# Optimization experiments

Hardware: AMD Instinct MI355X
Metric: run time of the kernel (lower is better)

Reference implementation:

```python
import jax, jax.numpy as jnp
import numpy as np

HEAD = 16
EPS = 1.1920929e-07  # torch.finfo(float32).eps, used by nn.RMSNorm when eps=None


def _rms(x, g):
    return x * jax.lax.rsqrt(jnp.mean(x * x, axis=-1, keepdims=True) + EPS) * g


def _heads(t):
    b, L, dm = t.shape
    return t.reshape(b, L, HEAD, dm // HEAD).transpose(0, 2, 1, 3)  # b h L d


def setup_inputs() -> dict:
    key = jax.random.key(0)
    ks = jax.random.split(key, 8)
    b, L, dims = 1, 1024, 1024
    s = dims ** -0.5
    x = jax.random.normal(ks[0], (b, L, dims), jnp.float32)
    pt = jax.random.normal(ks[1], (b, L, dims), jnp.float32)
    # additive causal mask (finite large-negative to stay grad-safe)
    mask = jnp.triu(jnp.full((L, L), -1e9, jnp.float32), k=1)
    return {
        "x": x, "pt": pt, "mask": mask,
        "gq": jnp.ones((dims,), jnp.float32),
        "Wq": jax.random.normal(ks[2], (dims, dims), jnp.float32) * s,
        "bq": jnp.zeros((dims,), jnp.float32),
        "gkv": jnp.ones((dims,), jnp.float32),
        "Wkv": jax.random.normal(ks[3], (dims, 2 * dims), jnp.float32) * s,
        "bkv": jnp.zeros((2 * dims,), jnp.float32),
        "gc": jnp.ones((dims,), jnp.float32),
        "Wc": jax.random.normal(ks[4], (dims, dims), jnp.float32) * s,
        "bc": jnp.zeros((dims,), jnp.float32),
        "Wout": jax.random.normal(ks[5], (dims, dims), jnp.float32) * s,
        "bout": jnp.zeros((dims,), jnp.float32),
        "context_window": 16,
    }


def reference(x, pt, mask, gq, Wq, bq, gkv, Wkv, bkv, gc, Wc, bc, Wout, bout, context_window):
    b, L, dims = x.shape
    d = dims // HEAD
    q = _heads(_rms(x, gq) @ Wq + bq)                      # b h L d
    kv = (_rms(x, gkv) @ Wkv + bkv).reshape(b, L, 2, HEAD, d)
    k = kv[:, :, 0].transpose(0, 2, 1, 3)                  # b h L d
    v = kv[:, :, 1].transpose(0, 2, 1, 3)
    c = _heads(_rms(pt, gc) @ Wc + bc)                     # b h L d

    # triplet_scores[i,j] = sum_{t=max(0,min(i,j)-w)}^{min(L,max(i,j)+w)-1} q_i . (k_j * c_t)
    # Vectorize with prefix sums over c: window sum = P[end] - P[start],
    # where end depends only on max(i,j) and start only on min(i,j).
    P = jnp.concatenate([jnp.zeros((b, HEAD, 1, d), x.dtype), jnp.cumsum(c, axis=2)], axis=2)  # b h L+1 d
    idx = jnp.arange(L)
    S = jnp.clip(idx - context_window, 0, L)   # start for min-index
    E = jnp.clip(idx + context_window, 0, L)   # end for max-index
    PE = jnp.take(P, E, axis=2)                # b h L d
    PS = jnp.take(P, S, axis=2)

    U = jnp.einsum('bhid,bhjd->bhij', q, k * PE)        # end from j (i<=j branch)
    V = jnp.einsum('bhid,bhjd->bhij', q * PS, k)        # start from i (i<=j branch)
    U2 = jnp.einsum('bhid,bhjd->bhij', q * PE, k)       # end from i (i>j branch)
    V2 = jnp.einsum('bhid,bhjd->bhij', q, k * PS)       # start from j (i>j branch)
    lower = idx[:, None] <= idx[None, :]
    triplet = jnp.where(lower, U - V, U2 - V2)          # b h L L

    scale = d ** -0.5
    qk = jnp.einsum('bhid,bhjd->bhij', q, k) * scale + triplet + mask[:L, :L]
    attn = jax.nn.softmax(qk, axis=-1)
    wv = jnp.einsum('bhij,bhjd->bhid', attn, v)
    out = wv.transpose(0, 2, 1, 3).reshape(b, L, dims) @ Wout + bout  # dropout p=0.01 is identity at eval
    return out
```

## Files before the change

### kernel.cpp

```cpp
#include <hip/hip_runtime.h>

#define LQ 1024
#define DM 1024


typedef __attribute__((ext_vector_type(8))) short bf16x8;
typedef __attribute__((ext_vector_type(4))) float f32x4;

#define MFMA(a, b, c) __builtin_amdgcn_mfma_f32_16x16x32_bf16((a), (b), (c), 0, 0, 0)
#define WAIT_LDS() __builtin_amdgcn_s_waitcnt(0xC07F)

__device__ __forceinline__ unsigned short f2bf(float x) {
    unsigned int u = __float_as_uint(x);
    return (unsigned short)((u + 0x7FFFu + ((u >> 16) & 1u)) >> 16);
}
__device__ __forceinline__ float bf2f(unsigned short h) {
    return __uint_as_float(((unsigned int)h) << 16);
}
__device__ __forceinline__ void gload16(const void* gp, void* lp) {
    __builtin_amdgcn_global_load_lds(
        (const __attribute__((address_space(1))) void*)gp,
        (__attribute__((address_space(3))) void*)lp, 16, 0, 0);
}
__device__ __forceinline__ void store_split4(unsigned short* ph, unsigned short* pl,
                                             float4 v) {
    unsigned short h0 = f2bf(v.x), h1 = f2bf(v.y), h2 = f2bf(v.z), h3 = f2bf(v.w);
    uint2 a;
    a.x = (unsigned)h0 | ((unsigned)h1 << 16);
    a.y = (unsigned)h2 | ((unsigned)h3 << 16);
    *(uint2*)ph = a;
    unsigned short l0 = f2bf(v.x - bf2f(h0)), l1 = f2bf(v.y - bf2f(h1));
    unsigned short l2 = f2bf(v.z - bf2f(h2)), l3 = f2bf(v.w - bf2f(h3));
    uint2 b;
    b.x = (unsigned)l0 | ((unsigned)l1 << 16);
    b.y = (unsigned)l2 | ((unsigned)l3 << 16);
    *(uint2*)pl = b;
}

__device__ __forceinline__ void rms_body(
    int row, const float* __restrict__ x, const float* __restrict__ pt,
    const float* __restrict__ gq, const float* __restrict__ gkv,
    const float* __restrict__ gc,
    unsigned short* xqn_h, unsigned short* xqn_l,
    unsigned short* xkvn_h, unsigned short* xkvn_l,
    unsigned short* ptn_h, unsigned short* ptn_l)
{
    const int t = threadIdx.x;
    const bool isx = row < LQ;
    const float* src = isx ? (x + (size_t)row * DM)
                           : (pt + (size_t)(row - LQ) * DM);
    float4 v = ((const float4*)src)[t];
    float ss = v.x*v.x + v.y*v.y + v.z*v.z + v.w*v.w;
    #pragma unroll
    for (int o = 32; o > 0; o >>= 1) ss += __shfl_down(ss, o);
    __shared__ float red[4];
    if ((t & 63) == 0) red[t >> 6] = ss;
    __syncthreads();
    const float r = rsqrtf((red[0] + red[1] + red[2] + red[3]) * (1.0f / DM)
                           + 1.1920929e-07f);
    const size_t base = (size_t)(isx ? row : row - LQ) * DM + t * 4;
    if (isx) {
        float4 g1 = ((const float4*)gq)[t];
        float4 g2 = ((const float4*)gkv)[t];
        float4 y1, y2;
        y1.x = v.x*r*g1.x; y1.y = v.y*r*g1.y; y1.z = v.z*r*g1.z; y1.w = v.w*r*g1.w;
        y2.x = v.x*r*g2.x; y2.y = v.y*r*g2.y; y2.z = v.z*r*g2.z; y2.w = v.w*r*g2.w;
        store_split4(xqn_h + base, xqn_l + base, y1);
        store_split4(xkvn_h + base, xkvn_l + base, y2);
    } else {
        float4 g = ((const float4*)gc)[t];
        float4 y;
        y.x = v.x*r*g.x; y.y = v.y*r*g.y; y.z = v.z*r*g.z; y.w = v.w*r*g.w;
        store_split4(ptn_h + base, ptn_l + base, y);
    }
}

__device__ __forceinline__ void wsplit_body(
    const float* __restrict__ in, unsigned short* oh, unsigned short* ol,
    int K, int N, int bx, int by)
{
    __shared__ float T[64 * 65];
    const int t = threadIdx.x;
    const int tx = t & 15, ty = t >> 4;
    const int c0 = bx * 64, r0 = by * 64;
    #pragma unroll
    for (int p = 0; p < 4; ++p) {
        int row = ty + p * 16;
        float4 v = *(const float4*)(in + (size_t)(r0 + row) * N + c0 + tx * 4);
        T[row * 65 + tx * 4 + 0] = v.x;
        T[row * 65 + tx * 4 + 1] = v.y;
        T[row * 65 + tx * 4 + 2] = v.z;
        T[row * 65 + tx * 4 + 3] = v.w;
    }
    __syncthreads();
    #pragma unroll
    for (int p = 0; p < 4; ++p) {
        int n = ty + p * 16;
        float4 w;
        w.x = T[(tx * 4 + 0) * 65 + n];
        w.y = T[(tx * 4 + 1) * 65 + n];
        w.z = T[(tx * 4 + 2) * 65 + n];
        w.w = T[(tx * 4 + 3) * 65 + n];
        size_t o = (size_t)(c0 + n) * K + r0 + tx * 4;
        store_split4(oh + o, ol + o, w);
    }
}

__global__ __launch_bounds__(256) void prep_kernel(
    const float* __restrict__ x, const float* __restrict__ pt,
    const float* __restrict__ gq, const float* __restrict__ gkv,
    const float* __restrict__ gc,
    const float* __restrict__ Wq, const float* __restrict__ Wkv,
    const float* __restrict__ Wc, const float* __restrict__ Wout,
    unsigned short* xqn_h, unsigned short* xqn_l,
    unsigned short* xkvn_h, unsigned short* xkvn_l,
    unsigned short* ptn_h, unsigned short* ptn_l,
    unsigned short* WqT_h, unsigned short* WqT_l,
    unsigned short* WkvT_h, unsigned short* WkvT_l,
    unsigned short* WcT_h, unsigned short* WcT_l,
    unsigned short* WoT_h, unsigned short* WoT_l)
{
    const int b = blockIdx.x;
    if (b < 2048) {
        rms_body(b, x, pt, gq, gkv, gc, xqn_h, xqn_l, xkvn_h, xkvn_l, ptn_h, ptn_l);
    } else if (b < 2304) {
        int s = b - 2048; wsplit_body(Wq, WqT_h, WqT_l, 1024, 1024, s & 15, s >> 4);
    } else if (b < 2816) {
        int s = b - 2304; wsplit_body(Wkv, WkvT_h, WkvT_l, 1024, 2048, s & 31, s >> 5);
    } else if (b < 3072) {
        int s = b - 2816; wsplit_body(Wc, WcT_h, WcT_l, 1024, 1024, s & 15, s >> 4);
    } else {
        int s = b - 3072; wsplit_body(Wout, WoT_h, WoT_l, 1024, 1024, s & 15, s >> 4);
    }
}

__device__ __forceinline__ void gemm3p(
    const unsigned short* __restrict__ Ah, const unsigned short* __restrict__ Al,
    const unsigned short* __restrict__ Bh, const unsigned short* __restrict__ Bl,
    const float* __restrict__ bias, float* __restrict__ out, int N, int mt, int nt)
{
    __shared__ unsigned short sAh[128 * 32], sAl[128 * 32];
    __shared__ unsigned short sBh[64 * 32], sBl[64 * 32];
    const int t = threadIdx.x;
    const int lane = t & 63, w = t >> 6;
    const int wm = w >> 1, wn = w & 1;
    const int n16 = lane & 15, quad = lane >> 4;
    const int srow = t >> 2, scol = (t & 3) * 8;
    f32x4 zero = {0.f, 0.f, 0.f, 0.f};
    f32x4 acc[4][2];
    #pragma unroll
    for (int ms = 0; ms < 4; ++ms)
        #pragma unroll
        for (int ns = 0; ns < 2; ++ns) acc[ms][ns] = zero;

    for (int kt = 0; kt < 32; ++kt) {
        const int k0 = kt * 32;
        __syncthreads();
        #pragma unroll
        for (int p = 0; p < 2; ++p) {
            const size_t ga = (size_t)(mt * 128 + srow + p * 64) * 1024 + k0 + scol;
            const int lb = w * 512 + p * 2048;
            gload16(Ah + ga, sAh + lb);
            gload16(Al + ga, sAl + lb);
        }
        {
            const size_t gb = (size_t)(nt * 64 + srow) * 1024 + k0 + scol;
            gload16(Bh + gb, sBh + w * 512);
            gload16(Bl + gb, sBl + w * 512);
        }
        __syncthreads();
        bf16x8 afh[4], afl[4], bfh[2], bfl[2];
        #pragma unroll
        for (int ms = 0; ms < 4; ++ms) {
            int r = wm * 64 + ms * 16 + n16;
            afh[ms] = *(const bf16x8*)&sAh[r * 32 + quad * 8];
            afl[ms] = *(const bf16x8*)&sAl[r * 32 + quad * 8];
        }
        #pragma unroll
        for (int ns = 0; ns < 2; ++ns) {
            int r = wn * 32 + ns * 16 + n16;
            bfh[ns] = *(const bf16x8*)&sBh[r * 32 + quad * 8];
            bfl[ns] = *(const bf16x8*)&sBl[r * 32 + quad * 8];
        }
        #pragma unroll
        for (int ms = 0; ms < 4; ++ms)
            #pragma unroll
            for (int ns = 0; ns < 2; ++ns) {
                acc[ms][ns] = MFMA(afh[ms], bfh[ns], acc[ms][ns]);
                acc[ms][ns] = MFMA(afh[ms], bfl[ns], acc[ms][ns]);
                acc[ms][ns] = MFMA(afl[ms], bfh[ns], acc[ms][ns]);
            }
    }
    #pragma unroll
    for (int ns = 0; ns < 2; ++ns) {
        const int col = nt * 64 + wn * 32 + ns * 16 + n16;
        const float bv = bias[col];
        #pragma unroll
        for (int ms = 0; ms < 4; ++ms) {
            const int row0 = mt * 128 + wm * 64 + ms * 16 + quad * 4;
            #pragma unroll
            for (int reg = 0; reg < 4; ++reg)
                out[(size_t)(row0 + reg) * N + col] = acc[ms][ns][reg] + bv;
        }
    }
}

__global__ __launch_bounds__(256) void proj_kernel(
    const unsigned short* __restrict__ xqn_h, const unsigned short* __restrict__ xqn_l,
    const unsigned short* __restrict__ xkvn_h, const unsigned short* __restrict__ xkvn_l,
    const unsigned short* __restrict__ ptn_h, const unsigned short* __restrict__ ptn_l,
    const unsigned short* __restrict__ WqT_h, const unsigned short* __restrict__ WqT_l,
    const unsigned short* __restrict__ WkvT_h, const unsigned short* __restrict__ WkvT_l,
    const unsigned short* __restrict__ WcT_h, const unsigned short* __restrict__ WcT_l,
    const float* __restrict__ bq, const float* __restrict__ bkv,
    const float* __restrict__ bc,
    float* __restrict__ Qb, float* __restrict__ KVb, float* __restrict__ Cb)
{
    const int bid = blockIdx.x;
    if (bid < 128) {
        gemm3p(xqn_h, xqn_l, WqT_h, WqT_l, bq, Qb, 1024, bid >> 4, bid & 15);
    } else if (bid < 384) {
        int b2 = bid - 128;
        gemm3p(xkvn_h, xkvn_l, WkvT_h, WkvT_l, bkv, KVb, 2048, b2 >> 5, b2 & 31);
    } else {
        int b2 = bid - 384;
        gemm3p(ptn_h, ptn_l, WcT_h, WcT_l, bc, Cb, 1024, b2 >> 4, b2 & 15);
    }
}

__global__ __launch_bounds__(256) void csum_kernel(const float* __restrict__ Cb,
                                                   float* __restrict__ csum)
{
    const int cid = blockIdx.x >> 2;
    const int col = ((blockIdx.x & 3) << 8) + threadIdx.x;
    const float* p = Cb + (size_t)cid * 32 * 1024 + col;
    float s = 0.f;
    #pragma unroll 8
    for (int r = 0; r < 32; ++r) s += p[(size_t)r * 1024];
    csum[cid * 1024 + col] = s;
}

__global__ __launch_bounds__(256) void scanp_kernel(const float* __restrict__ Cb,
                                                    const float* __restrict__ csum,
                                                    float* __restrict__ Pb)
{
    const int cid = blockIdx.x >> 2;
    const int col = ((blockIdx.x & 3) << 8) + threadIdx.x;
    float run = 0.f;
    for (int c = 0; c < cid; ++c) run += csum[c * 1024 + col];
    const float* p = Cb + (size_t)cid * 32 * 1024 + col;
    float* q = Pb + (size_t)cid * 32 * 1024 + col;
    for (int r = 0; r < 32; ++r) {
        q[(size_t)r * 1024] = run;
        run += p[(size_t)r * 1024];
    }
    if (cid == 31) Pb[(size_t)1024 * 1024 + col] = run;
}

__global__ __launch_bounds__(256) void abv_kernel(
    const float* __restrict__ Qb, const float* __restrict__ KVb,
    const float* __restrict__ Pb, const int* __restrict__ cwp,
    unsigned short* __restrict__ Aah, unsigned short* __restrict__ Aal,
    unsigned short* __restrict__ Bah, unsigned short* __restrict__ Bal,
    unsigned short* __restrict__ VT)
{
    const int b = blockIdx.x;
    if (b < 4096) {
        const int gid = b * 256 + threadIdx.x;
        const int i = gid >> 10;
        const int col = gid & 1023;
        const int h = col >> 6, dd = col & 63;
        const int cw = *cwp;
        const int E = min(i + cw, LQ);
        const int S = max(i - cw, 0);
        const float pe = Pb[(size_t)E * 1024 + col];
        const float ps = Pb[(size_t)S * 1024 + col];
        const float q = Qb[gid];
        const float k = KVb[(size_t)i * 2048 + col];
        const float scale = 0.125f;
        const size_t base = ((size_t)(h * 1024 + i)) * 128;
        float a0 = q, a1 = q * pe;
        float b0 = k * (scale - ps), b1 = k;
        unsigned short hv;
        hv = f2bf(a0); Aah[base + dd] = hv;      Aal[base + dd] = f2bf(a0 - bf2f(hv));
        hv = f2bf(a1); Aah[base + 64 + dd] = hv; Aal[base + 64 + dd] = f2bf(a1 - bf2f(hv));
        hv = f2bf(b0); Bah[base + dd] = hv;      Bal[base + dd] = f2bf(b0 - bf2f(hv));
        hv = f2bf(b1); Bah[base + 64 + dd] = hv; Bal[base + 64 + dd] = f2bf(b1 - bf2f(hv));
    } else {
        const int s = b - 4096;
        const int h = s >> 4, j0 = (s & 15) * 64;
        __shared__ float T[64 * 65];
        const int t = threadIdx.x;
        const int tx = t & 15, ty = t >> 4;
        #pragma unroll
        for (int p = 0; p < 4; ++p) {
            int j = ty + p * 16;
            float4 v = *(const float4*)(KVb + (size_t)(j0 + j) * 2048 + 1024 + h * 64 + tx * 4);
            T[j * 65 + tx * 4 + 0] = v.x;
            T[j * 65 + tx * 4 + 1] = v.y;
            T[j * 65 + tx * 4 + 2] = v.z;
            T[j * 65 + tx * 4 + 3] = v.w;
        }
        __syncthreads();
        #pragma unroll
        for (int p = 0; p < 4; ++p) {
            int d = ty + p * 16;
            unsigned short e0 = f2bf(T[(tx * 4 + 0) * 65 + d]);
            unsigned short e1 = f2bf(T[(tx * 4 + 1) * 65 + d]);
            unsigned short e2 = f2bf(T[(tx * 4 + 2) * 65 + d]);
            unsigned short e3 = f2bf(T[(tx * 4 + 3) * 65 + d]);
            uint2 pk;
            pk.x = (unsigned)e0 | ((unsigned)e1 << 16);
            pk.y = (unsigned)e2 | ((unsigned)e3 << 16);
            *(uint2*)(VT + (size_t)(h * 64 + d) * 1024 + j0 + tx * 4) = pk;
        }
    }
}

__global__ __launch_bounds__(256, 2) void attn_kernel(
    const unsigned short* __restrict__ Aah, const unsigned short* __restrict__ Aal,
    const unsigned short* __restrict__ Bah, const unsigned short* __restrict__ Bal,
    const unsigned short* __restrict__ VT,
    unsigned short* __restrict__ wvh, unsigned short* __restrict__ wvl)
{
    __shared__ unsigned short PsAll[4][16 * 68];
    __shared__ float cO[4][16 * 68];
    __shared__ float cM[4][16], cL[4][16];

    const int t = threadIdx.x;
    const int lane = t & 63, wid = t >> 6;
    unsigned short* Ps = PsAll[wid];
    const int b = blockIdx.x;
    const int h = b & 15;
    const int q = (b >> 4) & 15;
    const int group = b >> 8;
    const int it16 = (group == 0) ? q : (group == 1) ? (31 - q)
                   : (group == 2) ? (32 + q) : (63 - q);
    const int i0 = it16 * 16;
    const int njt = (i0 >> 6) + 1;
    const int n16 = lane & 15, quad = lane >> 4;

    bf16x8 afh[4], afl[4];
    {
        const size_t ar = ((size_t)(h * 1024 + i0 + n16)) * 128 + quad * 8;
        #pragma unroll
        for (int kc = 0; kc < 4; ++kc) {
            afh[kc] = *(const bf16x8*)(Aah + ar + kc * 32);
            afl[kc] = *(const bf16x8*)(Aal + ar + kc * 32);
        }
    }

    f32x4 zero = {0.f, 0.f, 0.f, 0.f};
    f32x4 oacc[4];
    #pragma unroll
    for (int dt = 0; dt < 4; ++dt) oacc[dt] = zero;
    float mrow[4], lrow[4];
    #pragma unroll
    for (int reg = 0; reg < 4; ++reg) { mrow[reg] = -1e30f; lrow[reg] = 0.f; }

    for (int jt = wid; jt < njt; jt += 4) {
        const int j0 = jt * 64;

        bf16x8 bh[4][4], bl[4][4];
        #pragma unroll
        for (int jj = 0; jj < 4; ++jj) {
            const size_t br = ((size_t)(h * 1024 + j0 + jj * 16 + n16)) * 128 + quad * 8;
            #pragma unroll
            for (int kc = 0; kc < 4; ++kc) {
                bh[jj][kc] = *(const bf16x8*)(Bah + br + kc * 32);
                bl[jj][kc] = *(const bf16x8*)(Bal + br + kc * 32);
            }
        }

        f32x4 s[4];
        #pragma unroll
        for (int jj = 0; jj < 4; ++jj) s[jj] = zero;
        #pragma unroll
        for (int jj = 0; jj < 4; ++jj)
            #pragma unroll
            for (int kc = 0; kc < 4; ++kc) {
                s[jj] = MFMA(afh[kc], bh[jj][kc], s[jj]);
                s[jj] = MFMA(afh[kc], bl[jj][kc], s[jj]);
                s[jj] = MFMA(afl[kc], bh[jj][kc], s[jj]);
            }

        if (jt == njt - 1) {
            const int ibase = i0 + quad * 4;
            #pragma unroll
            for (int jj = 0; jj < 4; ++jj) {
                const int j = j0 + jj * 16 + n16;
                #pragma unroll
                for (int reg = 0; reg < 4; ++reg)
                    if (j > ibase + reg) s[jj][reg] = -1e30f;
            }
        }

        float alpha[4];
        #pragma unroll
        for (int reg = 0; reg < 4; ++reg) {
            float mt_ = fmaxf(fmaxf(s[0][reg], s[1][reg]), fmaxf(s[2][reg], s[3][reg]));
            mt_ = fmaxf(mt_, __shfl_xor(mt_, 1));
            mt_ = fmaxf(mt_, __shfl_xor(mt_, 2));
            mt_ = fmaxf(mt_, __shfl_xor(mt_, 4));
            mt_ = fmaxf(mt_, __shfl_xor(mt_, 8));
            const float mn = fmaxf(mrow[reg], mt_);
            alpha[reg] = __expf(mrow[reg] - mn);
            mrow[reg] = mn;
            float rs = 0.f;
            #pragma unroll
            for (int jj = 0; jj < 4; ++jj) {
                float p = __expf(s[jj][reg] - mn);
                s[jj][reg] = p;
                rs += p;
            }
            rs += __shfl_xor(rs, 1); rs += __shfl_xor(rs, 2);
            rs += __shfl_xor(rs, 4); rs += __shfl_xor(rs, 8);
            lrow[reg] = lrow[reg] * alpha[reg] + rs;
        }

        WAIT_LDS();
        #pragma unroll
        for (int jj = 0; jj < 4; ++jj)
            #pragma unroll
            for (int reg = 0; reg < 4; ++reg)
                Ps[(quad * 4 + reg) * 68 + jj * 16 + n16] = f2bf(s[jj][reg]);
        WAIT_LDS();
        bf16x8 pf0 = *(const bf16x8*)&Ps[n16 * 68 + quad * 8];
        bf16x8 pf1 = *(const bf16x8*)&Ps[n16 * 68 + 32 + quad * 8];

        #pragma unroll
        for (int dt = 0; dt < 4; ++dt) {
            #pragma unroll
            for (int reg = 0; reg < 4; ++reg) oacc[dt][reg] *= alpha[reg];
            const size_t vr = ((size_t)(h * 64 + dt * 16 + n16)) * 1024 + j0 + quad * 8;
            bf16x8 vf0 = *(const bf16x8*)(VT + vr);
            bf16x8 vf1 = *(const bf16x8*)(VT + vr + 32);
            oacc[dt] = MFMA(pf0, vf0, oacc[dt]);
            oacc[dt] = MFMA(pf1, vf1, oacc[dt]);
        }
    }

    #pragma unroll
    for (int dt = 0; dt < 4; ++dt)
        #pragma unroll
        for (int reg = 0; reg < 4; ++reg)
            cO[wid][(quad * 4 + reg) * 68 + dt * 16 + n16] = oacc[dt][reg];
    if (n16 == 0) {
        #pragma unroll
        for (int reg = 0; reg < 4; ++reg) {
            cM[wid][quad * 4 + reg] = mrow[reg];
            cL[wid][quad * 4 + reg] = lrow[reg];
        }
    }
    __syncthreads();
    #pragma unroll
    for (int u = 0; u < 4; ++u) {
        const int p = u * 256 + t;
        const int r = p >> 6, d = p & 63;
        const float m0 = cM[0][r], m1 = cM[1][r], m2 = cM[2][r], m3 = cM[3][r];
        const float M = fmaxf(fmaxf(m0, m1), fmaxf(m2, m3));
        const float e0 = __expf(m0 - M), e1 = __expf(m1 - M);
        const float e2 = __expf(m2 - M), e3 = __expf(m3 - M);
        const float L = e0 * cL[0][r] + e1 * cL[1][r] + e2 * cL[2][r] + e3 * cL[3][r];
        const float o = e0 * cO[0][r * 68 + d] + e1 * cO[1][r * 68 + d]
                      + e2 * cO[2][r * 68 + d] + e3 * cO[3][r * 68 + d];
        const float v = o / L;
        const size_t oi = (size_t)(i0 + r) * 1024 + h * 64 + d;
        const unsigned short hv = f2bf(v);
        wvh[oi] = hv;
        wvl[oi] = f2bf(v - bf2f(hv));
    }
}

__global__ __launch_bounds__(128) void outgemm_kernel(
    const unsigned short* __restrict__ Ah, const unsigned short* __restrict__ Al,
    const unsigned short* __restrict__ Bh, const unsigned short* __restrict__ Bl,
    const float* __restrict__ bias, float* __restrict__ out)
{
    __shared__ unsigned short sAh[64 * 32], sAl[64 * 32];
    __shared__ unsigned short sBh[32 * 32], sBl[32 * 32];
    const int t = threadIdx.x;
    const int lane = t & 63, w = t >> 6;
    const int n16 = lane & 15, quad = lane >> 4;
    const int mt = blockIdx.x >> 5, nt = blockIdx.x & 31;
    const int srow = t >> 2, scol = (t & 3) * 8;
    f32x4 zero = {0.f, 0.f, 0.f, 0.f};
    f32x4 acc[2][2];
    #pragma unroll
    for (int ms = 0; ms < 2; ++ms)
        #pragma unroll
        for (int ns = 0; ns < 2; ++ns) acc[ms][ns] = zero;

    for (int kt = 0; kt < 32; ++kt) {
        const int k0 = kt * 32;
        __syncthreads();
        #pragma unroll
        for (int p = 0; p < 2; ++p) {
            const size_t ga = (size_t)(mt * 64 + srow + p * 32) * 1024 + k0 + scol;
            const int lb = w * 512 + p * 1024;
            gload16(Ah + ga, sAh + lb);
            gload16(Al + ga, sAl + lb);
        }
        {
            const size_t gb = (size_t)(nt * 32 + srow) * 1024 + k0 + scol;
            gload16(Bh + gb, sBh + w * 512);
            gload16(Bl + gb, sBl + w * 512);
        }
        __syncthreads();
        bf16x8 ah[2], al[2], bh[2], bl[2];
        #pragma unroll
        for (int ms = 0; ms < 2; ++ms) {
            int r = w * 32 + ms * 16 + n16;
            ah[ms] = *(const bf16x8*)&sAh[r * 32 + quad * 8];
            al[ms] = *(const bf16x8*)&sAl[r * 32 + quad * 8];
        }
        #pragma unroll
        for (int ns = 0; ns < 2; ++ns) {
            int r = ns * 16 + n16;
            bh[ns] = *(const bf16x8*)&sBh[r * 32 + quad * 8];
            bl[ns] = *(const bf16x8*)&sBl[r * 32 + quad * 8];
        }
        #pragma unroll
        for (int ms = 0; ms < 2; ++ms)
            #pragma unroll
            for (int ns = 0; ns < 2; ++ns) {
                acc[ms][ns] = MFMA(ah[ms], bh[ns], acc[ms][ns]);
                acc[ms][ns] = MFMA(ah[ms], bl[ns], acc[ms][ns]);
                acc[ms][ns] = MFMA(al[ms], bh[ns], acc[ms][ns]);
            }
    }
    #pragma unroll
    for (int ns = 0; ns < 2; ++ns) {
        const int col = nt * 32 + ns * 16 + n16;
        const float bv = bias[col];
        #pragma unroll
        for (int ms = 0; ms < 2; ++ms) {
            const int row0 = mt * 64 + w * 32 + ms * 16 + quad * 4;
            #pragma unroll
            for (int reg = 0; reg < 4; ++reg)
                out[(size_t)(row0 + reg) * 1024 + col] = acc[ms][ns][reg] + bv;
        }
    }
}

extern "C" void kernel_launch(void* const* d_in, const int* in_sizes, int n_in,
                              void* d_out, int out_size, void* d_ws, size_t ws_size,
                              hipStream_t stream) {
    (void)in_sizes; (void)n_in; (void)out_size; (void)ws_size;
    const float* x    = (const float*)d_in[0];
    const float* pt   = (const float*)d_in[1];
    const float* gq   = (const float*)d_in[3];
    const float* Wq   = (const float*)d_in[4];
    const float* bq   = (const float*)d_in[5];
    const float* gkv  = (const float*)d_in[6];
    const float* Wkv  = (const float*)d_in[7];
    const float* bkv  = (const float*)d_in[8];
    const float* gc   = (const float*)d_in[9];
    const float* Wc   = (const float*)d_in[10];
    const float* bc   = (const float*)d_in[11];
    const float* Wout = (const float*)d_in[12];
    const float* bout = (const float*)d_in[13];
    const int*   cw   = (const int*)d_in[14];
    float* out = (float*)d_out;

    char* W = (char*)d_ws;
    const size_t MB = 1u << 20;
    #define US(off) ((unsigned short*)(W + (size_t)(off)))
    #define FP(off) ((float*)(W + (size_t)(off)))
    unsigned short* xqn_h  = US(0 * MB);
    unsigned short* xqn_l  = US(2 * MB);
    unsigned short* xkvn_h = US(4 * MB);
    unsigned short* xkvn_l = US(6 * MB);
    unsigned short* ptn_h  = US(8 * MB);
    unsigned short* ptn_l  = US(10 * MB);
    unsigned short* WqT_h  = US(12 * MB);
    unsigned short* WqT_l  = US(14 * MB);
    unsigned short* WkvT_h = US(16 * MB);
    unsigned short* WkvT_l = US(20 * MB);
    unsigned short* WcT_h  = US(24 * MB);
    unsigned short* WcT_l  = US(26 * MB);
    unsigned short* WoT_h  = US(28 * MB);
    unsigned short* WoT_l  = US(30 * MB);
    float* Qb   = FP(32 * MB);
    float* KVb  = FP(36 * MB);
    float* Cb   = FP(44 * MB);
    float* Pb   = FP(48 * MB);
    float* csum = FP(52 * MB + 256 * 1024);
    unsigned short* Aah = US(0 * MB);
    unsigned short* Aal = US(4 * MB);
    unsigned short* Bah = US(8 * MB);
    unsigned short* Bal = US(12 * MB);
    unsigned short* VTb = US(16 * MB);
    unsigned short* wv_h = US(18 * MB);
    unsigned short* wv_l = US(20 * MB);
    #undef US
    #undef FP

    hipLaunchKernelGGL(prep_kernel, dim3(3328), dim3(256), 0, stream,
                       x, pt, gq, gkv, gc, Wq, Wkv, Wc, Wout,
                       xqn_h, xqn_l, xkvn_h, xkvn_l, ptn_h, ptn_l,
                       WqT_h, WqT_l, WkvT_h, WkvT_l, WcT_h, WcT_l, WoT_h, WoT_l);
    hipLaunchKernelGGL(proj_kernel, dim3(512), dim3(256), 0, stream,
                       xqn_h, xqn_l, xkvn_h, xkvn_l, ptn_h, ptn_l,
                       WqT_h, WqT_l, WkvT_h, WkvT_l, WcT_h, WcT_l,
                       bq, bkv, bc, Qb, KVb, Cb);
    hipLaunchKernelGGL(csum_kernel, dim3(128), dim3(256), 0, stream, Cb, csum);
    hipLaunchKernelGGL(scanp_kernel, dim3(128), dim3(256), 0, stream, Cb, csum, Pb);
    hipLaunchKernelGGL(abv_kernel, dim3(4352), dim3(256), 0, stream,
                       Qb, KVb, Pb, cw, Aah, Aal, Bah, Bal, VTb);
    hipLaunchKernelGGL(attn_kernel, dim3(1024), dim3(256), 0, stream,
                       Aah, Aal, Bah, Bal, VTb, wv_h, wv_l);
    hipLaunchKernelGGL(outgemm_kernel, dim3(512), dim3(128), 0, stream,
                       wv_h, wv_l, WoT_h, WoT_l, bout, out);
}
```

Before: 223.1 us.

## Use single-wave 64x64 projection GEMM tiles and reverse attention block order

Replaces the 256-thread 128x64 projection GEMM with a one-wavefront 64x64 tile per block. Each wave loads its own LDS tiles and needs no block barriers, and it issues the next k-step's global-to-LDS loads right after reading the current fragments, so they overlap the MFMAs. The grid doubles to 1024 blocks for more parallelism, at the cost of more redundant global loads per output. The attention kernel's row-tile order is also reversed so the longest causal tiles are scheduled first, to improve load balance.

```diff
diff --git a/kernel.cpp b/kernel.cpp
--- a/kernel.cpp
+++ b/kernel.cpp
@@ -9,6 +9,7 @@
 
 #define MFMA(a, b, c) __builtin_amdgcn_mfma_f32_16x16x32_bf16((a), (b), (c), 0, 0, 0)
 #define WAIT_LDS() __builtin_amdgcn_s_waitcnt(0xC07F)
+#define WAIT_VM()  __builtin_amdgcn_s_waitcnt(0x0F70)
 
 __device__ __forceinline__ unsigned short f2bf(float x) {
     unsigned int u = __float_as_uint(x);
@@ -134,70 +135,77 @@
     }
 }
 
-__device__ __forceinline__ void gemm3p(
+__device__ __forceinline__ void stage1w(
+    const unsigned short* __restrict__ Ah, const unsigned short* __restrict__ Al,
+    const unsigned short* __restrict__ Bh, const unsigned short* __restrict__ Bl,
+    size_t abase, size_t bbase, int k0, int srow, int scol,
+    unsigned short* sAh, unsigned short* sAl,
+    unsigned short* sBh, unsigned short* sBl)
+{
+    #pragma unroll
+    for (int p = 0; p < 4; ++p) {
+        const size_t ga = abase + (size_t)(p * 16 + srow) * 1024 + k0 + scol;
+        const size_t gb = bbase + (size_t)(p * 16 + srow) * 1024 + k0 + scol;
+        gload16(Ah + ga, sAh + p * 512);
+        gload16(Al + ga, sAl + p * 512);
+        gload16(Bh + gb, sBh + p * 512);
+        gload16(Bl + gb, sBl + p * 512);
+    }
+}
+
+__device__ __forceinline__ void gemm1w(
     const unsigned short* __restrict__ Ah, const unsigned short* __restrict__ Al,
     const unsigned short* __restrict__ Bh, const unsigned short* __restrict__ Bl,
     const float* __restrict__ bias, float* __restrict__ out, int N, int mt, int nt)
 {
-    __shared__ unsigned short sAh[128 * 32], sAl[128 * 32];
+    __shared__ unsigned short sAh[64 * 32], sAl[64 * 32];
     __shared__ unsigned short sBh[64 * 32], sBl[64 * 32];
-    const int t = threadIdx.x;
-    const int lane = t & 63, w = t >> 6;
-    const int wm = w >> 1, wn = w & 1;
+    const int lane = threadIdx.x;
     const int n16 = lane & 15, quad = lane >> 4;
-    const int srow = t >> 2, scol = (t & 3) * 8;
+    const int srow = lane >> 2, scol = (lane & 3) * 8;
+
     f32x4 zero = {0.f, 0.f, 0.f, 0.f};
-    f32x4 acc[4][2];
+    f32x4 acc[4][4];
     #pragma unroll
     for (int ms = 0; ms < 4; ++ms)
         #pragma unroll
-        for (int ns = 0; ns < 2; ++ns) acc[ms][ns] = zero;
-
+        for (int ns = 0; ns < 4; ++ns) acc[ms][ns] = zero;
+
+    const size_t abase = (size_t)(mt * 64) * 1024;
+    const size_t bbase = (size_t)(nt * 64) * 1024;
+
+    stage1w(Ah, Al, Bh, Bl, abase, bbase, 0, srow, scol, sAh, sAl, sBh, sBl);
     for (int kt = 0; kt < 32; ++kt) {
-        const int k0 = kt * 32;
-        __syncthreads();
-        #pragma unroll
-        for (int p = 0; p < 2; ++p) {
-            const size_t ga = (size_t)(mt * 128 + srow + p * 64) * 1024 + k0 + scol;
-            const int lb = w * 512 + p * 2048;
-            gload16(Ah + ga, sAh + lb);
-            gload16(Al + ga, sAl + lb);
-        }
-        {
-            const size_t gb = (size_t)(nt * 64 + srow) * 1024 + k0 + scol;
-            gload16(Bh + gb, sBh + w * 512);
-            gload16(Bl + gb, sBl + w * 512);
-        }
-        __syncthreads();
-        bf16x8 afh[4], afl[4], bfh[2], bfl[2];
-        #pragma unroll
-        for (int ms = 0; ms < 4; ++ms) {
-            int r = wm * 64 + ms * 16 + n16;
-            afh[ms] = *(const bf16x8*)&sAh[r * 32 + quad * 8];
-            afl[ms] = *(const bf16x8*)&sAl[r * 32 + quad * 8];
-        }
-        #pragma unroll
-        for (int ns = 0; ns < 2; ++ns) {
-            int r = wn * 32 + ns * 16 + n16;
-            bfh[ns] = *(const bf16x8*)&sBh[r * 32 + quad * 8];
-            bfl[ns] = *(const bf16x8*)&sBl[r * 32 + quad * 8];
-        }
+        WAIT_VM();
+        bf16x8 afh[4], afl[4], bfh[4], bfl[4];
+        #pragma unroll
+        for (int i = 0; i < 4; ++i) {
+            const int ro = (i * 16 + n16) * 32 + quad * 8;
+            afh[i] = *(const bf16x8*)&sAh[ro];
+            afl[i] = *(const bf16x8*)&sAl[ro];
+            bfh[i] = *(const bf16x8*)&sBh[ro];
+            bfl[i] = *(const bf16x8*)&sBl[ro];
+        }
+        WAIT_LDS();
+        if (kt < 31)
+            stage1w(Ah, Al, Bh, Bl, abase, bbase, (kt + 1) * 32, srow, scol,
+                    sAh, sAl, sBh, sBl);
         #pragma unroll
         for (int ms = 0; ms < 4; ++ms)
             #pragma unroll
-            for (int ns = 0; ns < 2; ++ns) {
+            for (int ns = 0; ns < 4; ++ns) {
                 acc[ms][ns] = MFMA(afh[ms], bfh[ns], acc[ms][ns]);
                 acc[ms][ns] = MFMA(afh[ms], bfl[ns], acc[ms][ns]);
                 acc[ms][ns] = MFMA(afl[ms], bfh[ns], acc[ms][ns]);
             }
     }
     #pragma unroll
-    for (int ns = 0; ns < 2; ++ns) {
-        const int col = nt * 64 + wn * 32 + ns * 16 + n16;
+    for (int ns = 0; ns < 4; ++ns) {
+        const int col = nt * 64 + ns * 16 + n16;
         const float bv = bias[col];
         #pragma unroll
         for (int ms = 0; ms < 4; ++ms) {
-            const int row0 = mt * 128 + wm * 64 + ms * 16 + quad * 4;
+            const int row0 = mt * 64 + ms * 16 + quad * 4;
             #pragma unroll
             for (int reg = 0; reg < 4; ++reg)
                 out[(size_t)(row0 + reg) * N + col] = acc[ms][ns][reg] + bv;
@@ -205,7 +213,7 @@
     }
 }
 
-__global__ __launch_bounds__(256) void proj_kernel(
+__global__ __launch_bounds__(64) void proj_kernel(
     const unsigned short* __restrict__ xqn_h, const unsigned short* __restrict__ xqn_l,
     const unsigned short* __restrict__ xkvn_h, const unsigned short* __restrict__ xkvn_l,
     const unsigned short* __restrict__ ptn_h, const unsigned short* __restrict__ ptn_l,
@@ -217,14 +225,14 @@
     float* __restrict__ Qb, float* __restrict__ KVb, float* __restrict__ Cb)
 {
     const int bid = blockIdx.x;
-    if (bid < 128) {
-        gemm3p(xqn_h, xqn_l, WqT_h, WqT_l, bq, Qb, 1024, bid >> 4, bid & 15);
-    } else if (bid < 384) {
-        int b2 = bid - 128;
-        gemm3p(xkvn_h, xkvn_l, WkvT_h, WkvT_l, bkv, KVb, 2048, b2 >> 5, b2 & 31);
+    if (bid < 256) {
+        gemm1w(xqn_h, xqn_l, WqT_h, WqT_l, bq, Qb, 1024, bid >> 4, bid & 15);
+    } else if (bid < 768) {
+        int b2 = bid - 256;
+        gemm1w(xkvn_h, xkvn_l, WkvT_h, WkvT_l, bkv, KVb, 2048, b2 >> 5, b2 & 31);
     } else {
-        int b2 = bid - 384;
-        gemm3p(ptn_h, ptn_l, WcT_h, WcT_l, bc, Cb, 1024, b2 >> 4, b2 & 15);
+        int b2 = bid - 768;
+        gemm1w(ptn_h, ptn_l, WcT_h, WcT_l, bc, Cb, 1024, b2 >> 4, b2 & 15);
     }
 }
 
@@ -334,8 +342,8 @@
     const int h = b & 15;
     const int q = (b >> 4) & 15;
     const int group = b >> 8;
-    const int it16 = (group == 0) ? q : (group == 1) ? (31 - q)
-                   : (group == 2) ? (32 + q) : (63 - q);
+    const int it16 = (group == 0) ? (63 - q) : (group == 1) ? (32 + q)
+                   : (group == 2) ? (31 - q) : q;
     const int i0 = it16 * 16;
     const int njt = (i0 >> 6) + 1;
     const int n16 = lane & 15, quad = lane >> 4;
@@ -600,7 +608,7 @@
                        x, pt, gq, gkv, gc, Wq, Wkv, Wc, Wout,
                        xqn_h, xqn_l, xkvn_h, xkvn_l, ptn_h, ptn_l,
                        WqT_h, WqT_l, WkvT_h, WkvT_l, WcT_h, WcT_l, WoT_h, WoT_l);
-    hipLaunchKernelGGL(proj_kernel, dim3(512), dim3(256), 0, stream,
+    hipLaunchKernelGGL(proj_kernel, dim3(1024), dim3(64), 0, stream,
                        xqn_h, xqn_l, xkvn_h, xkvn_l, ptn_h, ptn_l,
                        WqT_h, WqT_l, WkvT_h, WkvT_l, WcT_h, WcT_l,
                        bq, bkv, bc, Qb, KVb, Cb);
```

Result: slower. 236.7 us (+6.1%).
